# Optimization experiments

Measured on AMD Instinct MI355X. Metric: run time of the kernel, lower is better.

## Reference

```python
import jax, jax.numpy as jnp
import numpy as np

H = 16; KV = 4; D = 128; HID = 2048; MAX_POS = 4096; RANK = 8; ALPHA = 16.0; THETA = 10000.0


def _lora_dense(x, kernel, a, b):
    # base kernel path is stop-gradient'd in the original LoRADense
    x = x.astype(jnp.bfloat16)
    y = x @ jax.lax.stop_gradient(kernel.astype(jnp.bfloat16))
    y = y + (ALPHA / RANK) * ((x @ a.astype(jnp.bfloat16)) @ b.astype(jnp.bfloat16))
    return y.astype(jnp.float32)


def _apply_rope(xq, xk, position_ids):
    # complex rotation expressed with real cos/sin on interleaved (even, odd) pairs
    dt = xq.dtype
    xq = xq.astype(jnp.bfloat16).astype(jnp.float32)
    xk = xk.astype(jnp.bfloat16).astype(jnp.float32)
    d = xq.shape[-1]
    inv_freq = 1.0 / THETA ** (jnp.arange(0, d, 2)[: d // 2].astype(jnp.float32) / d)
    angles = jnp.arange(MAX_POS, dtype=jnp.float32)[:, None] * inv_freq[None, :]  # (max_pos, d/2)
    cos = jnp.cos(angles)[position_ids][:, :, None, :]  # (b, s, 1, d/2)
    sin = jnp.sin(angles)[position_ids][:, :, None, :]

    def rot(x):
        xe = x[..., 0::2]
        xo = x[..., 1::2]
        re = xe * cos - xo * sin
        im = xe * sin + xo * cos
        return jnp.stack((re, im), axis=-1).reshape(x.shape)

    return rot(xq).astype(dt), rot(xk).astype(dt)


def _forward(hidden_states, attention_mask, position_ids, wq_kernel, wq_a, wq_b,
             wk_kernel, wk_a, wk_b, wv_kernel, wv_a, wv_b, wo_kernel, wo_a, wo_b):
    b, s, _ = hidden_states.shape
    hs = hidden_states.astype(jnp.bfloat16)
    xq = _lora_dense(hs, wq_kernel, wq_a, wq_b).reshape(b, s, H, D)
    g = H // KV
    # GQA: repeat each kv head g times along the head axis ('b s (h d) -> b s (h g) d')
    xk = jnp.repeat(_lora_dense(hs, wk_kernel, wk_a, wk_b).reshape(b, s, KV, D), g, axis=2)
    xv = jnp.repeat(_lora_dense(hs, wv_kernel, wv_a, wv_b).reshape(b, s, KV, D), g, axis=2)
    xq, xk = _apply_rope(xq, xk, position_ids)
    causal = jnp.tril(jnp.ones((s, s), dtype=bool))
    mask = attention_mask[:, None, None, :] & causal[None, None]  # (b, 1, q, k)
    bias = jnp.where(mask, 0.0, jnp.finfo(jnp.float32).min)
    scale = 1.0 / np.sqrt(D).astype(np.float32)
    scores = jnp.einsum('bqhd,bkhd->bhqk', (xq * scale).astype(jnp.bfloat16),
                        xk.astype(jnp.bfloat16)).astype(jnp.float32) + bias
    attn = jax.nn.softmax(scores, axis=-1)
    out = jnp.einsum('bhqk,bkhd->bqhd', attn, xv).reshape(b, s, H * D)
    return _lora_dense(out, wo_kernel, wo_a, wo_b)


def setup_inputs():
    key = jax.random.key(0)
    ks = jax.random.split(key, 16)
    B, S = 2, 2048
    w = lambda k, shp, sc=0.02: jax.random.normal(k, shp, dtype=jnp.float32) * sc
    return {
        'hidden_states': jax.random.normal(ks[0], (B, S, HID), dtype=jnp.float32),
        'attention_mask': jnp.ones((B, S), dtype=bool),
        'position_ids': jnp.broadcast_to(jnp.arange(S, dtype=jnp.int32), (B, S)),
        'wq_kernel': w(ks[1], (HID, H * D)),
        'wq_a': w(ks[2], (HID, RANK), 0.01),
        'wq_b': w(ks[3], (RANK, H * D), 0.01),
        'wk_kernel': w(ks[4], (HID, KV * D)),
        'wk_a': w(ks[5], (HID, RANK), 0.01),
        'wk_b': w(ks[6], (RANK, KV * D), 0.01),
        'wv_kernel': w(ks[7], (HID, KV * D)),
        'wv_a': w(ks[8], (HID, RANK), 0.01),
        'wv_b': w(ks[9], (RANK, KV * D), 0.01),
        'wo_kernel': w(ks[10], (H * D, HID)),
        'wo_a': w(ks[11], (H * D, RANK), 0.01),
        'wo_b': w(ks[12], (RANK, HID), 0.01),
    }


def reference(hidden_states, attention_mask, position_ids, wq_kernel, wq_a, wq_b,
              wk_kernel, wk_a, wk_b, wv_kernel, wv_a, wv_b, wo_kernel, wo_a, wo_b):
    return _forward(hidden_states, attention_mask, position_ids, wq_kernel, wq_a, wq_b,
                    wk_kernel, wk_a, wk_b, wv_kernel, wv_a, wv_b, wo_kernel, wo_a, wo_b)
```

## Files before the change

kernel.cpp:

```cpp
#include <hip/hip_runtime.h>
#include <hip/hip_bf16.h>
#include <cstdint>

#define H_    16
#define KV_   4
#define D_    128
#define HID_  2048
#define B_    2
#define S_    2048
#define NROW_ (B_*S_)
#define HD_   (H_*D_)
#define KVD_  (KV_*D_)
#define NQKV_ (HD_ + 2*KVD_)
#define SCALE_ 0.08838834764831843f
#define L2E_   1.44269504088896f
#define QSC_   (SCALE_ * L2E_)
#define THR2_  11.5415603f
#define NEG_  -1e30f

typedef float  f32x4  __attribute__((ext_vector_type(4)));
typedef __bf16 bf16x8 __attribute__((ext_vector_type(8)));
typedef __bf16 bf16x4 __attribute__((ext_vector_type(4)));

__device__ __forceinline__ unsigned short f2bf(float x) {
  unsigned u = __float_as_uint(x);
  return (unsigned short)((u + 0x7FFFu + ((u >> 16) & 1u)) >> 16);
}
__device__ __forceinline__ float bf2f(unsigned short h) {
  return __uint_as_float(((unsigned)h) << 16);
}

__device__ __forceinline__ void glds16(const void* g, void* l) {
  typedef __attribute__((address_space(1))) const char G;
  typedef __attribute__((address_space(3))) char L;
  __builtin_amdgcn_global_load_lds((const G*)(unsigned long long)g,
                                   (L*)(unsigned)(unsigned long long)l, 16, 0, 0);
}

__global__ __launch_bounds__(256) void fold_all(
    const float* __restrict__ wq, const float* __restrict__ wqa, const float* __restrict__ wqb,
    const float* __restrict__ wk, const float* __restrict__ wka, const float* __restrict__ wkb,
    const float* __restrict__ wv, const float* __restrict__ wva, const float* __restrict__ wvb,
    const float* __restrict__ wo, const float* __restrict__ woa, const float* __restrict__ wob,
    unsigned short* __restrict__ Wqkv, unsigned short* __restrict__ Wot) {
  const int z = blockIdx.z;
  const float *W, *A, *Bm; unsigned short* Wt; int N;
  if (z == 0)      { W = wq; A = wqa; Bm = wqb; Wt = Wqkv;                         N = 2048; }
  else if (z == 1) { W = wk; A = wka; Bm = wkb; Wt = Wqkv + (size_t)2048 * 2048;   N = 512;  }
  else if (z == 2) { W = wv; A = wva; Bm = wvb; Wt = Wqkv + (size_t)2560 * 2048;   N = 512;  }
  else             { W = wo; A = woa; Bm = wob; Wt = Wot;                          N = 2048; }
  const int K = 2048;
  const int k0 = blockIdx.x << 6, n0 = blockIdx.y << 6;
  if (n0 >= N) return;

  __shared__ float Bs[8 * 64];
  __shared__ unsigned short tt[64 * 72];
  const int tid = threadIdx.x;
#pragma unroll
  for (int i = 0; i < 2; ++i) {
    int c = i * 256 + tid;
    Bs[c] = bf2f(f2bf(Bm[(c >> 6) * N + n0 + (c & 63)]));
  }
  __syncthreads();
  const int kr = tid >> 2, nc = (tid & 3) << 4;
  float a[8];
#pragma unroll
  for (int r = 0; r < 8; ++r) a[r] = 2.0f * bf2f(f2bf(A[(k0 + kr) * 8 + r]));
#pragma unroll
  for (int i = 0; i < 4; ++i) {
    float4 wv4 = *(const float4*)(W + (size_t)(k0 + kr) * N + n0 + nc + i * 4);
    float e[4] = {wv4.x, wv4.y, wv4.z, wv4.w};
#pragma unroll
    for (int q = 0; q < 4; ++q) {
      int n = nc + i * 4 + q;
      float acc = bf2f(f2bf(e[q]));
#pragma unroll
      for (int r = 0; r < 8; ++r) acc += a[r] * Bs[r * 64 + n];
      tt[kr * 72 + n] = f2bf(acc);
    }
  }
  __syncthreads();
  const int nr = tid >> 2, kc = (tid & 3) << 4;
#pragma unroll
  for (int i = 0; i < 2; ++i) {
    unsigned short o[8];
#pragma unroll
    for (int e2 = 0; e2 < 8; ++e2) o[e2] = tt[(kc + i * 8 + e2) * 72 + nr];
    *(bf16x8*)(Wt + (size_t)(n0 + nr) * K + k0 + kc + i * 8) = *(const bf16x8*)o;
  }
}

__global__ __launch_bounds__(256) void castrig(const float* __restrict__ in,
                                               unsigned short* __restrict__ out,
                                               float* __restrict__ tab) {
  const int bx = blockIdx.x, tid = threadIdx.x;
  if (bx < 8192) {
    int i = bx * 256 + tid;
    float4 v = ((const float4*)in)[i];
    ushort4 o; o.x = f2bf(v.x); o.y = f2bf(v.y); o.z = f2bf(v.z); o.w = f2bf(v.w);
    ((ushort4*)out)[i] = o;
  } else {
    int p = (bx - 8192) * 4 + (tid >> 6);
    int j = tid & 63;
    float invf = __powf(10000.0f, -(float)j / 64.0f);
    float a = (float)p * invf;
    float s, c;
    sincosf(a, &s, &c);
    tab[(p * 64 + j) * 2 + 0] = c;
    tab[(p * 64 + j) * 2 + 1] = s;
  }
}

__global__ __launch_bounds__(256) void ropevt(unsigned short* __restrict__ QKV,
                                              const int* __restrict__ pos,
                                              const float* __restrict__ trig,
                                              unsigned short* __restrict__ VT) {
  __shared__ unsigned short t[64 * 65];
  const int bx = blockIdx.x, tid = threadIdx.x;
  if (bx < 2560) {
    int gid = bx * 256 + tid;
    int row = gid / 160;
    int ch = gid - row * 160;
    bool isq = ch < 128;
    int col = isq ? (ch << 4) : (HD_ + ((ch - 128) << 4));
    int j0 = (isq ? (ch & 7) : ((ch - 128) & 7)) << 3;
    int pp = pos[row];
    const float* tb = trig + ((size_t)pp * 64 + j0) * 2;
    float4 t0 = *(const float4*)(tb);
    float4 t1 = *(const float4*)(tb + 4);
    float4 t2 = *(const float4*)(tb + 8);
    float4 t3 = *(const float4*)(tb + 12);
    float cc[8] = {t0.x, t0.z, t1.x, t1.z, t2.x, t2.z, t3.x, t3.z};
    float ss[8] = {t0.y, t0.w, t1.y, t1.w, t2.y, t2.w, t3.y, t3.w};
    unsigned short* base = QKV + (size_t)row * NQKV_ + col;
    unsigned short xin[16], xo[16];
    *(bf16x8*)xin = *(const bf16x8*)base;
    *(bf16x8*)(xin + 8) = *(const bf16x8*)(base + 8);
    float scl = isq ? QSC_ : 1.0f;
#pragma unroll
    for (int p = 0; p < 8; ++p) {
      float x0 = bf2f(xin[2 * p]), x1 = bf2f(xin[2 * p + 1]);
      float re = (x0 * cc[p] - x1 * ss[p]) * scl;
      float im = (x0 * ss[p] + x1 * cc[p]) * scl;
      xo[2 * p] = f2bf(re); xo[2 * p + 1] = f2bf(im);
    }
    *(bf16x8*)base = *(const bf16x8*)xo;
    *(bf16x8*)(base + 8) = *(const bf16x8*)(xo + 8);
  } else {
    const int bb = bx - 2560;
    const int s0 = (bb & 31) << 6, d0 = ((bb >> 5) & 1) << 6;
    const int bk = bb >> 6, b = bk >> 2, hkv = bk & 3;
#pragma unroll
    for (int i = 0; i < 2; ++i) {
      int c = i * 256 + tid;
      int sr = c >> 3, c8 = c & 7;
      bf16x8 v = *(const bf16x8*)(QKV + (size_t)(b * S_ + s0 + sr) * NQKV_
                                  + HD_ + KVD_ + hkv * D_ + d0 + c8 * 8);
      const unsigned short* u = (const unsigned short*)&v;
#pragma unroll
      for (int k = 0; k < 8; ++k) t[sr * 65 + c8 * 8 + k] = u[k];
    }
    __syncthreads();
#pragma unroll
    for (int i = 0; i < 2; ++i) {
      int c = i * 256 + tid;
      int dr = c >> 3, c8 = c & 7;
      unsigned short o[8];
#pragma unroll
      for (int k = 0; k < 8; ++k) o[k] = t[(c8 * 8 + k) * 65 + dr];
      *(bf16x8*)(VT + ((size_t)(bk * 128 + d0 + dr)) * S_ + s0 + c8 * 8) =
          *(const bf16x8*)o;
    }
  }
}

template <int BN, int OUTF32>
__global__ __launch_bounds__(512, 1) void gemm8p(const unsigned short* __restrict__ A,
                                                 const unsigned short* __restrict__ Bt,
                                                 void* __restrict__ C,
                                                 int M, int N, int K) {
  constexpr int ASLAB = 256 * 64;
  constexpr int BSLAB = BN * 64;
  constexpr int NFR = BN / 64;
  constexpr int WCOL = BN / 4;
  __shared__ __align__(16) unsigned short lds[3 * ASLAB + 2 * BSLAB];
  unsigned short* const ldsB = lds + 3 * ASLAB;
  const int tid = threadIdx.x, lane = tid & 63, w = tid >> 6;
  const int g = lane >> 4, l15 = lane & 15;
  const int wm = w >> 2, wn = w & 3;

  const int x = blockIdx.x & 7, inner = blockIdx.x >> 3;
  const int bm = (x >> 1) * 4 + (inner >> 3);
  const int bn = (x & 1) * 8 + (inner & 7);
  const int row0 = bm << 8, col0 = bn * BN;
  const int nkt = K >> 6;

  auto stA = [&](int kt, int slab, int part) {
    if (kt < nkt) {
#pragma unroll
      for (int j = 0; j < 2; ++j) {
        int jj = part * 2 + j;
        int c = jj * 512 + tid;
        int r = c >> 3, s = c & 7, slot = s ^ (r & 7);
        glds16(A + (size_t)(row0 + r) * K + (kt << 6) + slot * 8,
               (char*)(lds + slab * ASLAB) + (size_t)(jj * 512 + w * 64) * 16);
      }
    }
  };
  auto stB = [&](int kt, int slab, int part) {
    if (kt < nkt) {
      constexpr int split = (NFR == 3) ? 2 : 1;
      const int jlo = part ? split : 0;
      const int jhi = part ? NFR : split;
#pragma unroll
      for (int jj = 0; jj < NFR; ++jj) {
        if (jj >= jlo && jj < jhi) {
          int c = jj * 512 + tid;
          int r = c >> 3, s = c & 7, slot = s ^ (r & 7);
          glds16(Bt + (size_t)(col0 + r) * K + (kt << 6) + slot * 8,
                 (char*)(ldsB + slab * BSLAB) + (size_t)(jj * 512 + w * 64) * 16);
        }
      }
    }
  };

  f32x4 acc[8][NFR];
#pragma unroll
  for (int i = 0; i < 8; ++i)
#pragma unroll
    for (int j = 0; j < NFR; ++j) acc[i][j] = (f32x4){0.f, 0.f, 0.f, 0.f};
  bf16x8 bfr[NFR][2];

  stB(0, 0, 0); stB(0, 0, 1);
  stA(0, 0, 0); stA(0, 0, 1);
  stA(1, 1, 0); stA(1, 1, 1);
  asm volatile("s_waitcnt vmcnt(0)" ::: "memory");
  __builtin_amdgcn_s_barrier();

  int am = 0;
  for (int kt = 0; kt < nkt; ++kt) {
    const unsigned short* bufA = lds + am * ASLAB;
    const unsigned short* bufB = ldsB + (kt & 1) * BSLAB;
    int as2 = am + 2; if (as2 >= 3) as2 -= 3;
    const int bs1 = (kt + 1) & 1;
#pragma unroll
    for (int q = 0; q < 4; ++q) {
      bf16x8 af[2][2];
#pragma unroll
      for (int mi = 0; mi < 2; ++mi) {
        int r = wm * 128 + q * 32 + mi * 16 + l15;
#pragma unroll
        for (int ks = 0; ks < 2; ++ks) {
          int slot = (ks * 4 + g) ^ (r & 7);
          af[mi][ks] = *(const bf16x8*)(bufA + r * 64 + slot * 8);
        }
      }
      if (q == 0) {
#pragma unroll
        for (int ni = 0; ni < NFR; ++ni) {
          int r = wn * WCOL + ni * 16 + l15;
#pragma unroll
          for (int ks = 0; ks < 2; ++ks) {
            int slot = (ks * 4 + g) ^ (r & 7);
            bfr[ni][ks] = *(const bf16x8*)(bufB + r * 64 + slot * 8);
          }
        }
      }
      if (q == 0)      stB(kt + 1, bs1, 0);
      else if (q == 1) stB(kt + 1, bs1, 1);
      else if (q == 2) stA(kt + 2, as2, 0);
      else {
        stA(kt + 2, as2, 1);
        if (kt + 2 < nkt) asm volatile("s_waitcnt vmcnt(4)" ::: "memory");
        else              asm volatile("s_waitcnt vmcnt(0)" ::: "memory");
      }
      __builtin_amdgcn_s_barrier();
      asm volatile("s_waitcnt lgkmcnt(0)" ::: "memory");
      __builtin_amdgcn_s_setprio(1);
#pragma unroll
      for (int ks = 0; ks < 2; ++ks)
#pragma unroll
        for (int mi = 0; mi < 2; ++mi)
#pragma unroll
          for (int ni = 0; ni < NFR; ++ni)
            acc[q * 2 + mi][ni] =
                __builtin_amdgcn_mfma_f32_16x16x32_bf16(af[mi][ks], bfr[ni][ks],
                                                        acc[q * 2 + mi][ni], 0, 0, 0);
      __builtin_amdgcn_s_setprio(0);
      __builtin_amdgcn_s_barrier();
    }
    am = (am + 1 == 3) ? 0 : am + 1;
  }

#pragma unroll
  for (int f = 0; f < 8; ++f)
#pragma unroll
    for (int jj = 0; jj < 4; ++jj) {
      int r = row0 + wm * 128 + f * 16 + g * 4 + jj;
#pragma unroll
      for (int ni = 0; ni < NFR; ++ni) {
        int cc = col0 + wn * WCOL + ni * 16 + l15;
        float v = acc[f][ni][jj];
        if (OUTF32) ((float*)C)[(size_t)r * N + cc] = v;
        else        ((unsigned short*)C)[(size_t)r * N + cc] = f2bf(v);
      }
    }
}

__global__ __launch_bounds__(256, 4) void attn_k(const unsigned short* __restrict__ QKV,
                                                 const unsigned short* __restrict__ VT,
                                                 unsigned short* __restrict__ O) {
  __shared__ __align__(16) unsigned short smem[37376];
  const int tid = threadIdx.x, lane = tid & 63, w = tid >> 6;
  const int g = lane >> 4, l15 = lane & 15;

  const int dd = blockIdx.x;
  const int grp = dd & 7;
  const int t64 = dd >> 3;
  const int pair = t64 & 15;
  const int bh = grp * 4 + (t64 >> 4);
  const int b = bh >> 4, h = bh & 15, hkv = (h >> 2);

  const unsigned short* QKVk0 = QKV + (size_t)b * S_ * NQKV_ + HD_ + hkv * D_;
  const unsigned short* VT0  = VT + (size_t)(b * 4 + hkv) * 128 * S_;

  int gk[4], gv[4], dsl[4];
#pragma unroll
  for (int i = 0; i < 4; ++i) {
    int c = i * 256 + w * 64 + lane;
    { int r = c >> 4, s = c & 15; gk[i] = r * NQKV_ + (s ^ (r & 7)) * 8; }
    { int d = c >> 3, s = c & 7;  gv[i] = d * S_ + (s ^ (d & 7)) * 8; }
    dsl[i] = (i * 256 + w * 64) * 16;
  }
  int koff[4][4], voff[2][8], pwo[4], pro[2];
#pragma unroll
  for (int ks = 0; ks < 4; ++ks)
#pragma unroll
    for (int m = 0; m < 4; ++m) {
      int r = m * 16 + l15;
      koff[ks][m] = r * 128 + ((ks * 4 + g) ^ (r & 7)) * 8;
    }
#pragma unroll
  for (int ks = 0; ks < 2; ++ks)
#pragma unroll
    for (int nd = 0; nd < 8; ++nd) {
      int d = nd * 16 + l15;
      voff[ks][nd] = d * 64 + ((ks * 4 + g) ^ (d & 7)) * 8;
    }
#pragma unroll
  for (int m = 0; m < 4; ++m) pwo[m] = l15 * 72 + m * 16 + g * 4;
#pragma unroll
  for (int ks = 0; ks < 2; ++ks) pro[ks] = l15 * 72 + ks * 32 + g * 8;
  const int PB = 32768 + w * 1152;
  char* const smemc = (char*)smem;

#define STAGE(KB, KOB, VOB) do {                                            \
    const unsigned short* bk_ = QKVk0 + (size_t)(KB) * NQKV_;               \
    const unsigned short* bv_ = VT0 + (KB);                                 \
    _Pragma("unroll")                                                       \
    for (int i_ = 0; i_ < 4; ++i_) {                                        \
      glds16(bk_ + gk[i_], smemc + (KOB) + dsl[i_]);                        \
      glds16(bv_ + gv[i_], smemc + (VOB) + dsl[i_]);                        \
    }                                                                       \
  } while (0)

#define COMPUTE(KOH, VOH, TCUR) do {                                        \
    f32x4 sacc[4];                                                          \
    _Pragma("unroll") for (int m = 0; m < 4; ++m)                           \
      sacc[m] = (f32x4){0.f, 0.f, 0.f, 0.f};                                \
    __builtin_amdgcn_s_setprio(1);                                          \
    _Pragma("unroll") for (int ks = 0; ks < 4; ++ks) {                      \
      bf16x8 kf[4];                                                         \
      _Pragma("unroll") for (int m = 0; m < 4; ++m)                         \
        kf[m] = *(const bf16x8*)(smem + (KOH) + koff[ks][m]);               \
      _Pragma("unroll") for (int m = 0; m < 4; ++m)                         \
        sacc[m] = __builtin_amdgcn_mfma_f32_16x16x32_bf16(kf[m], qf[ks], sacc[m], 0, 0, 0); \
    }                                                                       \
    __builtin_amdgcn_s_setprio(0);                                          \
    if ((TCUR) == qt) {                                                     \
      _Pragma("unroll") for (int m = 0; m < 4; ++m)                         \
        _Pragma("unroll") for (int jj = 0; jj < 4; ++jj)                    \
          if (m * 16 + g * 4 + jj > w * 16 + l15) sacc[m][jj] = NEG_;       \
    }                                                                       \
    float pm = NEG_;                                                        \
    _Pragma("unroll") for (int m = 0; m < 4; ++m)                           \
      _Pragma("unroll") for (int jj = 0; jj < 4; ++jj)                      \
        pm = fmaxf(pm, sacc[m][jj]);                                        \
    bool skip = __all(pm <= mrun + THR2_);                                  \
    float mnew;                                                             \
    if (skip) {                                                             \
      mnew = mrun;                                                          \
    } else {                                                                \
      pm = fmaxf(pm, __shfl_xor(pm, 16));                                   \
      pm = fmaxf(pm, __shfl_xor(pm, 32));                                   \
      mnew = fmaxf(mrun, pm);                                               \
    }                                                                       \
    float ls = 0.f;                                                         \
    _Pragma("unroll") for (int m = 0; m < 4; ++m)                           \
      _Pragma("unroll") for (int jj = 0; jj < 4; ++jj) {                    \
        float pv = __builtin_amdgcn_exp2f(sacc[m][jj] - mnew);              \
        sacc[m][jj] = pv;                                                   \
        ls += pv;                                                           \
      }                                                                     \
    _Pragma("unroll") for (int m = 0; m < 4; ++m) {                         \
      bf16x4 pk = {(__bf16)sacc[m][0], (__bf16)sacc[m][1],                  \
                   (__bf16)sacc[m][2], (__bf16)sacc[m][3]};                 \
      *(bf16x4*)(smem + PB + pwo[m]) = pk;                                  \
    }                                                                       \
    if (skip) {                                                             \
      lrun += ls;                                                           \
    } else {                                                                \
      float sc = __builtin_amdgcn_exp2f(mrun - mnew);                       \
      lrun = lrun * sc + ls;                                                \
      mrun = mnew;                                                          \
      _Pragma("unroll") for (int jj = 0; jj < 4; ++jj) {                    \
        int srcl = (lane & 48) | (g * 4 + jj);                              \
        float s = __shfl(sc, srcl);                                         \
        _Pragma("unroll") for (int nd = 0; nd < 8; ++nd) oacc[nd][jj] *= s; \
      }                                                                     \
    }                                                                       \
    __builtin_amdgcn_s_setprio(1);                                          \
    _Pragma("unroll") for (int ks = 0; ks < 2; ++ks) {                      \
      bf16x8 pf = *(const bf16x8*)(smem + PB + pro[ks]);                    \
      _Pragma("unroll") for (int nd = 0; nd < 8; ++nd) {                    \
        bf16x8 vf = *(const bf16x8*)(smem + (VOH) + voff[ks][nd]);          \
        oacc[nd] = __builtin_amdgcn_mfma_f32_16x16x32_bf16(pf, vf, oacc[nd], 0, 0, 0); \
      }                                                                     \
    }                                                                       \
    __builtin_amdgcn_s_setprio(0);                                          \
  } while (0)

  for (int qsel = 0; qsel < 2; ++qsel) {
    const int qt = qsel ? (31 - pair) : pair;
    const int q_base = qt << 6;
    const int ntile = qt + 1;

    bf16x8 qf[4];
#pragma unroll
    for (int ks = 0; ks < 4; ++ks)
      qf[ks] = *(const bf16x8*)(QKV + (size_t)(b * S_ + q_base + w * 16 + l15) * NQKV_
                                + h * D_ + ks * 32 + g * 8);

    f32x4 oacc[8];
#pragma unroll
    for (int nd = 0; nd < 8; ++nd) oacc[nd] = (f32x4){0.f, 0.f, 0.f, 0.f};
    float mrun = NEG_, lrun = 0.f;

    STAGE(0, 0, 32768);
    __syncthreads();
    for (int t = 0; t < ntile; t += 2) {
      const bool m1 = t + 1 < ntile;
      if (m1) STAGE((t + 1) << 6, 16384, 49152);
      COMPUTE(0, 16384, t);
      __syncthreads();
      if (!m1) break;
      if (t + 2 < ntile) STAGE((t + 2) << 6, 0, 32768);
      COMPUTE(8192, 24576, t + 1);
      __syncthreads();
    }

    lrun += __shfl_xor(lrun, 16);
    lrun += __shfl_xor(lrun, 32);

    float inv[4];
#pragma unroll
    for (int jj = 0; jj < 4; ++jj) {
      int srcl = (lane & 48) | (g * 4 + jj);
      inv[jj] = 1.0f / __shfl(lrun, srcl);
    }
    unsigned short* sE = smem;
#pragma unroll
    for (int nd = 0; nd < 8; ++nd)
#pragma unroll
      for (int jj = 0; jj < 4; ++jj) {
        __bf16 e = (__bf16)(oacc[nd][jj] * inv[jj]);
        sE[(w * 16 + g * 4 + jj) * 136 + nd * 16 + l15] = *(unsigned short*)&e;
      }
    __syncthreads();
#pragma unroll
    for (int i = 0; i < 4; ++i) {
      int c = i * 256 + tid;
      int r = c >> 4, c16 = c & 15;
      bf16x8 vv = *(const bf16x8*)(sE + r * 136 + c16 * 8);
      *(bf16x8*)(O + (size_t)(b * S_ + q_base + r) * HD_ + h * D_ + c16 * 8) = vv;
    }
    __syncthreads();
  }
#undef STAGE
#undef COMPUTE
}

extern "C" void kernel_launch(void* const* d_in, const int* in_sizes, int n_in,
                              void* d_out, int out_size, void* d_ws, size_t ws_size,
                              hipStream_t stream) {
  const float* hs  = (const float*)d_in[0];
  const int*   pos = (const int*)d_in[2];
  const float* wq  = (const float*)d_in[3];
  const float* wqa = (const float*)d_in[4];
  const float* wqb = (const float*)d_in[5];
  const float* wk  = (const float*)d_in[6];
  const float* wka = (const float*)d_in[7];
  const float* wkb = (const float*)d_in[8];
  const float* wv  = (const float*)d_in[9];
  const float* wva = (const float*)d_in[10];
  const float* wvb = (const float*)d_in[11];
  const float* wo  = (const float*)d_in[12];
  const float* woa = (const float*)d_in[13];
  const float* wob = (const float*)d_in[14];

  char* ws = (char*)d_ws;
  unsigned short* Xb   = (unsigned short*)(ws);
  unsigned short* Wqkv = (unsigned short*)(ws + 16777216);
  unsigned short* Wot  = (unsigned short*)(ws + 29360128);
  unsigned short* QKV  = (unsigned short*)(ws + 37748736);
  unsigned short* VT   = (unsigned short*)(ws + 62914560);
  float*          trig = (float*)(ws + 67108864);

  fold_all<<<dim3(32, 32, 4), 256, 0, stream>>>(wq, wqa, wqb, wk, wka, wkb,
                                                wv, wva, wvb, wo, woa, wob,
                                                Wqkv, Wot);
  castrig<<<8704, 256, 0, stream>>>(hs, Xb, trig);
  gemm8p<192, 0><<<256, 512, 0, stream>>>(Xb, Wqkv, QKV, 4096, 3072, 2048);
  ropevt<<<3072, 256, 0, stream>>>(QKV, pos, trig, VT);
  attn_k<<<512, 256, 0, stream>>>(QKV, VT, Xb );
  gemm8p<128, 1><<<256, 512, 0, stream>>>(Xb, Wot, d_out, 4096, 2048, 2048);
}
```

Before: 183.1 us.

## Share K/V tiles across the four GQA heads in one attention block

The attention kernel is restructured so each block handles a 32-row query tile for all four query heads that share a KV head, with 8 waves (2 row groups × 4 heads). K/V tiles staged in LDS are reused by four heads instead of one, cutting global K/V traffic per head. The old pair-balanced scheduling (pair and 31-pair tiles per block) is replaced by one tile per block, ordered longest-first, and the P buffer layout is swizzled to avoid LDS bank conflicts. Block size doubles to 512 threads, which changes occupancy and register pressure. Causal masking now uses absolute positions because 32-row query tiles no longer line up with 64-key tiles.

```diff
diff --git a/kernel.cpp b/kernel.cpp
--- a/kernel.cpp
+++ b/kernel.cpp
@@ -307,30 +307,33 @@
     }
 }
 
-__global__ __launch_bounds__(256, 4) void attn_k(const unsigned short* __restrict__ QKV,
+__global__ __launch_bounds__(512, 4) void attn_k(const unsigned short* __restrict__ QKV,
                                                  const unsigned short* __restrict__ VT,
                                                  unsigned short* __restrict__ O) {
-  __shared__ __align__(16) unsigned short smem[37376];
+  __shared__ __align__(16) unsigned short smem[40960];
   const int tid = threadIdx.x, lane = tid & 63, w = tid >> 6;
   const int g = lane >> 4, l15 = lane & 15;
+  const int wr = w & 1;
+  const int wh = w >> 1;
 
   const int dd = blockIdx.x;
   const int grp = dd & 7;
-  const int t64 = dd >> 3;
-  const int pair = t64 & 15;
-  const int bh = grp * 4 + (t64 >> 4);
-  const int b = bh >> 4, h = bh & 15, hkv = (h >> 2);
+  const int b = grp >> 2, hkv = grp & 3;
+  const int qt = 63 - (dd >> 3);
+  const int q_base = qt << 5;
+  const int ntile = (qt >> 1) + 1;
+  const int h = hkv * 4 + wh;
 
   const unsigned short* QKVk0 = QKV + (size_t)b * S_ * NQKV_ + HD_ + hkv * D_;
   const unsigned short* VT0  = VT + (size_t)(b * 4 + hkv) * 128 * S_;
 
-  int gk[4], gv[4], dsl[4];
-#pragma unroll
-  for (int i = 0; i < 4; ++i) {
-    int c = i * 256 + w * 64 + lane;
+  int gk[2], gv[2], dsl[2];
+#pragma unroll
+  for (int i = 0; i < 2; ++i) {
+    int c = i * 512 + tid;
     { int r = c >> 4, s = c & 15; gk[i] = r * NQKV_ + (s ^ (r & 7)) * 8; }
     { int d = c >> 3, s = c & 7;  gv[i] = d * S_ + (s ^ (d & 7)) * 8; }
-    dsl[i] = (i * 256 + w * 64) * 16;
+    dsl[i] = (i * 512 + w * 64) * 16;
   }
   int koff[4][4], voff[2][8], pwo[4], pro[2];
 #pragma unroll
@@ -348,17 +351,20 @@
       voff[ks][nd] = d * 64 + ((ks * 4 + g) ^ (d & 7)) * 8;
     }
 #pragma unroll
-  for (int m = 0; m < 4; ++m) pwo[m] = l15 * 72 + m * 16 + g * 4;
-#pragma unroll
-  for (int ks = 0; ks < 2; ++ks) pro[ks] = l15 * 72 + ks * 32 + g * 8;
-  const int PB = 32768 + w * 1152;
+  for (int m = 0; m < 4; ++m)
+    pwo[m] = l15 * 64 + ((2 * m + (g >> 1) + l15) & 7) * 8 + (g & 1) * 4;
+#pragma unroll
+  for (int ks = 0; ks < 2; ++ks)
+    pro[ks] = l15 * 64 + ((ks * 4 + g + l15) & 7) * 8;
+  const int PB = 32768 + w * 1024;
   char* const smemc = (char*)smem;
+  const int qg = q_base + wr * 16 + l15;
 
 #define STAGE(KB, KOB, VOB) do {                                            \
     const unsigned short* bk_ = QKVk0 + (size_t)(KB) * NQKV_;               \
     const unsigned short* bv_ = VT0 + (KB);                                 \
     _Pragma("unroll")                                                       \
-    for (int i_ = 0; i_ < 4; ++i_) {                                        \
+    for (int i_ = 0; i_ < 2; ++i_) {                                        \
       glds16(bk_ + gk[i_], smemc + (KOB) + dsl[i_]);                        \
       glds16(bv_ + gv[i_], smemc + (VOB) + dsl[i_]);                        \
     }                                                                       \
@@ -377,10 +383,11 @@
         sacc[m] = __builtin_amdgcn_mfma_f32_16x16x32_bf16(kf[m], qf[ks], sacc[m], 0, 0, 0); \
     }                                                                       \
     __builtin_amdgcn_s_setprio(0);                                          \
-    if ((TCUR) == qt) {                                                     \
+    if ((TCUR) == ntile - 1) {                                              \
+      const int kb_ = (TCUR) << 6;                                          \
       _Pragma("unroll") for (int m = 0; m < 4; ++m)                         \
         _Pragma("unroll") for (int jj = 0; jj < 4; ++jj)                    \
-          if (m * 16 + g * 4 + jj > w * 16 + l15) sacc[m][jj] = NEG_;       \
+          if (kb_ + m * 16 + g * 4 + jj > qg) sacc[m][jj] = NEG_;           \
     }                                                                       \
     float pm = NEG_;                                                        \
     _Pragma("unroll") for (int m = 0; m < 4; ++m)                           \
@@ -430,61 +437,54 @@
     __builtin_amdgcn_s_setprio(0);                                          \
   } while (0)
 
-  for (int qsel = 0; qsel < 2; ++qsel) {
-    const int qt = qsel ? (31 - pair) : pair;
-    const int q_base = qt << 6;
-    const int ntile = qt + 1;
-
-    bf16x8 qf[4];
-#pragma unroll
-    for (int ks = 0; ks < 4; ++ks)
-      qf[ks] = *(const bf16x8*)(QKV + (size_t)(b * S_ + q_base + w * 16 + l15) * NQKV_
-                                + h * D_ + ks * 32 + g * 8);
-
-    f32x4 oacc[8];
-#pragma unroll
-    for (int nd = 0; nd < 8; ++nd) oacc[nd] = (f32x4){0.f, 0.f, 0.f, 0.f};
-    float mrun = NEG_, lrun = 0.f;
-
-    STAGE(0, 0, 32768);
+  bf16x8 qf[4];
+#pragma unroll
+  for (int ks = 0; ks < 4; ++ks)
+    qf[ks] = *(const bf16x8*)(QKV + (size_t)(b * S_ + qg) * NQKV_
+                              + h * D_ + ks * 32 + g * 8);
+
+  f32x4 oacc[8];
+#pragma unroll
+  for (int nd = 0; nd < 8; ++nd) oacc[nd] = (f32x4){0.f, 0.f, 0.f, 0.f};
+  float mrun = NEG_, lrun = 0.f;
+
+  STAGE(0, 0, 32768);
+  __syncthreads();
+  for (int t = 0; t < ntile; t += 2) {
+    const bool m1 = t + 1 < ntile;
+    if (m1) STAGE((t + 1) << 6, 16384, 49152);
+    COMPUTE(0, 16384, t);
     __syncthreads();
-    for (int t = 0; t < ntile; t += 2) {
-      const bool m1 = t + 1 < ntile;
-      if (m1) STAGE((t + 1) << 6, 16384, 49152);
-      COMPUTE(0, 16384, t);
-      __syncthreads();
-      if (!m1) break;
-      if (t + 2 < ntile) STAGE((t + 2) << 6, 0, 32768);
-      COMPUTE(8192, 24576, t + 1);
-      __syncthreads();
-    }
-
-    lrun += __shfl_xor(lrun, 16);
-    lrun += __shfl_xor(lrun, 32);
-
-    float inv[4];
+    if (!m1) break;
+    if (t + 2 < ntile) STAGE((t + 2) << 6, 0, 32768);
+    COMPUTE(8192, 24576, t + 1);
+    __syncthreads();
+  }
+
+  lrun += __shfl_xor(lrun, 16);
+  lrun += __shfl_xor(lrun, 32);
+
+  float inv[4];
+#pragma unroll
+  for (int jj = 0; jj < 4; ++jj) {
+    int srcl = (lane & 48) | (g * 4 + jj);
+    inv[jj] = 1.0f / __shfl(lrun, srcl);
+  }
+  unsigned short* sE = smem + wh * 4352;
+#pragma unroll
+  for (int nd = 0; nd < 8; ++nd)
 #pragma unroll
     for (int jj = 0; jj < 4; ++jj) {
-      int srcl = (lane & 48) | (g * 4 + jj);
-      inv[jj] = 1.0f / __shfl(lrun, srcl);
-    }
-    unsigned short* sE = smem;
-#pragma unroll
-    for (int nd = 0; nd < 8; ++nd)
-#pragma unroll
-      for (int jj = 0; jj < 4; ++jj) {
-        __bf16 e = (__bf16)(oacc[nd][jj] * inv[jj]);
-        sE[(w * 16 + g * 4 + jj) * 136 + nd * 16 + l15] = *(unsigned short*)&e;
-      }
-    __syncthreads();
-#pragma unroll
-    for (int i = 0; i < 4; ++i) {
-      int c = i * 256 + tid;
-      int r = c >> 4, c16 = c & 15;
-      bf16x8 vv = *(const bf16x8*)(sE + r * 136 + c16 * 8);
-      *(bf16x8*)(O + (size_t)(b * S_ + q_base + r) * HD_ + h * D_ + c16 * 8) = vv;
-    }
-    __syncthreads();
+      __bf16 e = (__bf16)(oacc[nd][jj] * inv[jj]);
+      sE[(wr * 16 + g * 4 + jj) * 136 + nd * 16 + l15] = *(unsigned short*)&e;
+    }
+  __syncthreads();
+#pragma unroll
+  for (int i = 0; i < 4; ++i) {
+    int c = i * 512 + tid;
+    int hh2 = c >> 9, r = (c >> 4) & 31, c16 = c & 15;
+    bf16x8 vv = *(const bf16x8*)(smem + hh2 * 4352 + r * 136 + c16 * 8);
+    *(bf16x8*)(O + (size_t)(b * S_ + q_base + r) * HD_ + (hkv * 4 + hh2) * D_ + c16 * 8) = vv;
   }
 #undef STAGE
 #undef COMPUTE
@@ -522,6 +522,6 @@
   castrig<<<8704, 256, 0, stream>>>(hs, Xb, trig);
   gemm8p<192, 0><<<256, 512, 0, stream>>>(Xb, Wqkv, QKV, 4096, 3072, 2048);
   ropevt<<<3072, 256, 0, stream>>>(QKV, pos, trig, VT);
-  attn_k<<<512, 256, 0, stream>>>(QKV, VT, Xb );
+  attn_k<<<512, 512, 0, stream>>>(QKV, VT, Xb );
   gemm8p<128, 1><<<256, 512, 0, stream>>>(Xb, Wot, d_out, 4096, 2048, 2048);
 }
```

Measured after the change: 186.5 us. Within noise of the previous version (+1.9%).
